# Kernel tuning notes

Measured on AMD Instinct MI355X. Metric: run time of the kernel, lower is better.

## Reference

```python
import jax, jax.numpy as jnp
import numpy as np

# ----- config (mirrors SpatialAxis init) -----
B, N = 1, 32768
D_MODEL, NHEAD, DEPTH = 256, 8, 2
COORD = 3
PATCH = 512          # self.patch_size default
BITS = 10            # self.morton_bits default
SHIFT = True         # self.shift_order default
MLP_H = 4 * D_MODEL
HD = D_MODEL // NHEAD
EPS = 1e-5


def _part1by2(v):
    # spread low 10 bits of int32 so there are 2 zero bits between each
    v = v & 0x000003FF
    v = (v | (v << 16)) & 0x030000FF
    v = (v | (v << 8)) & 0x0300F00F
    v = (v | (v << 4)) & 0x030C30C3
    v = (v | (v << 2)) & 0x09249249
    return v


def _perm_for_block(coords, i):
    # Z-order (Morton) serialization with per-block axis rotation; odd blocks
    # shift the order by half a patch (shifted-window style). Returns [B,N] int32.
    c = jax.lax.stop_gradient(coords)[..., np.roll(np.arange(COORD), -i)]
    cmin = c.min(axis=1, keepdims=True)
    cmax = c.max(axis=1, keepdims=True)
    q = ((c - cmin) / (cmax - cmin + 1e-9) * (2 ** BITS - 1)).astype(jnp.int32)
    q = jnp.clip(q, 0, 2 ** BITS - 1)
    code = (_part1by2(q[..., 0]) | (_part1by2(q[..., 1]) << 1)
            | (_part1by2(q[..., 2]) << 2))  # [B,N]
    perm = jnp.argsort(code, axis=1)
    if SHIFT and (i % 2 == 1):
        perm = jnp.roll(perm, PATCH // 2, axis=1)
    return perm


def _ln(x, g, b):
    m = x.mean(-1, keepdims=True)
    v = x.var(-1, keepdims=True)
    return (x - m) * jax.lax.rsqrt(v + EPS) * g + b


def _point_block(xs, cs, p):
    # xs: [M, P, D] tokens of one patch each; cs: [M, P, 3]
    M, P, D = xs.shape
    h = _ln(xs, p['ln1_g'], p['ln1_b'])
    qkv = h @ p['w_qkv'] + p['b_qkv']                         # [M,P,3D]
    q, k, v = jnp.split(qkv, 3, axis=-1)
    q = q.reshape(M, P, NHEAD, HD)
    k = k.reshape(M, P, NHEAD, HD)
    v = v.reshape(M, P, NHEAD, HD)
    scores = jnp.einsum('mphd,mqhd->mhpq', q, k) / np.sqrt(HD).astype(np.float32)
    rel = cs[:, :, None, :] - cs[:, None, :, :]               # [M,P,P,3]
    bias = jnp.einsum('mpqc,ch->mhpq', rel, p['w_pos']) + p['b_pos'][None, :, None, None]
    attn = jax.nn.softmax(scores + bias, axis=-1)
    o = jnp.einsum('mhpq,mqhd->mphd', attn, v).reshape(M, P, D)
    xs = xs + o @ p['w_proj'] + p['b_proj']
    h2 = _ln(xs, p['ln2_g'], p['ln2_b'])
    xs = xs + jax.nn.gelu(h2 @ p['w_fc1'] + p['b_fc1']) @ p['w_fc2'] + p['b_fc2']
    return xs


def _forward(x, coords, params):
    Cc = coords.shape[-1]
    nblk = N // PATCH
    for i in range(DEPTH):
        p = {k: v[i] for k, v in params.items()}
        perm = _perm_for_block(coords, i)                      # [B,N]
        inv = jnp.argsort(perm, axis=1)
        x_s = jnp.take_along_axis(x, perm[:, :, None], axis=1)
        c_s = jnp.take_along_axis(coords, perm[:, :, None], axis=1)
        x_f = x_s.reshape(B * nblk, PATCH, D_MODEL)
        c_f = c_s.reshape(B * nblk, PATCH, Cc)
        y = _point_block(x_f, c_f, p).reshape(B, N, D_MODEL)
        x = jnp.take_along_axis(y, inv[:, :, None], axis=1)
    return _ln(x, params['norm_g'][0], params['norm_b'][0])


def setup_inputs() -> dict:
    key = jax.random.key(0)
    ks = jax.random.split(key, 20)
    s = 0.02
    d = {
        'x': jax.random.normal(ks[0], (B, N, D_MODEL), jnp.float32),
        'coords': jax.random.uniform(ks[1], (B, N, COORD), jnp.float32),
        'ln1_g': jnp.ones((DEPTH, D_MODEL), jnp.float32),
        'ln1_b': jnp.zeros((DEPTH, D_MODEL), jnp.float32),
        'w_qkv': jax.random.normal(ks[2], (DEPTH, D_MODEL, 3 * D_MODEL), jnp.float32) * s,
        'b_qkv': jnp.zeros((DEPTH, 3 * D_MODEL), jnp.float32),
        'w_proj': jax.random.normal(ks[3], (DEPTH, D_MODEL, D_MODEL), jnp.float32) * s,
        'b_proj': jnp.zeros((DEPTH, D_MODEL), jnp.float32),
        'w_pos': jax.random.normal(ks[4], (DEPTH, COORD, NHEAD), jnp.float32) * s,
        'b_pos': jnp.zeros((DEPTH, NHEAD), jnp.float32),
        'ln2_g': jnp.ones((DEPTH, D_MODEL), jnp.float32),
        'ln2_b': jnp.zeros((DEPTH, D_MODEL), jnp.float32),
        'w_fc1': jax.random.normal(ks[5], (DEPTH, D_MODEL, MLP_H), jnp.float32) * s,
        'b_fc1': jnp.zeros((DEPTH, MLP_H), jnp.float32),
        'w_fc2': jax.random.normal(ks[6], (DEPTH, MLP_H, D_MODEL), jnp.float32) * s,
        'b_fc2': jnp.zeros((DEPTH, D_MODEL), jnp.float32),
        'norm_g': jnp.ones((1, D_MODEL), jnp.float32),
        'norm_b': jnp.zeros((1, D_MODEL), jnp.float32),
    }
    return d


def reference(x, coords, ln1_g, ln1_b, w_qkv, b_qkv, w_proj, b_proj, w_pos, b_pos,
              ln2_g, ln2_b, w_fc1, b_fc1, w_fc2, b_fc2, norm_g, norm_b):
    params = dict(ln1_g=ln1_g, ln1_b=ln1_b, w_qkv=w_qkv, b_qkv=b_qkv,
                  w_proj=w_proj, b_proj=b_proj, w_pos=w_pos, b_pos=b_pos,
                  ln2_g=ln2_g, ln2_b=ln2_b, w_fc1=w_fc1, b_fc1=b_fc1,
                  w_fc2=w_fc2, b_fc2=b_fc2, norm_g=norm_g, norm_b=norm_b)
    return _forward(x, coords, params)
```

## Files before the change

kernel.cpp:

```cpp
#include <hip/hip_runtime.h>

typedef unsigned long long u64;
typedef unsigned int u32;
typedef unsigned short u16;
typedef float f32x4 __attribute__((ext_vector_type(4)));
typedef __bf16 bf16x8 __attribute__((ext_vector_type(8)));

#define N_TOK 32768

__device__ inline u16 f2bf(float f){
  u32 x = __float_as_uint(f);
  u32 r = x + 0x7FFFu + ((x >> 16) & 1u);
  return (u16)(r >> 16);
}

__device__ inline u16 f2bf_hw(float f){
  u32 pk;
  asm("v_cvt_pk_bf16_f32 %0, %1, %2" : "=v"(pk) : "v"(f), "v"(0.f));
  return (u16)pk;
}

__device__ inline f32x4 mfma16(bf16x8 a, bf16x8 b, f32x4 c){
  return __builtin_amdgcn_mfma_f32_16x16x32_bf16(a, b, c, 0, 0, 0);
}

__device__ inline float fexp2(float x){
  float r;
  asm("v_exp_f32 %0, %1" : "=v"(r) : "v"(x));
  return r;
}
__device__ inline float frcp(float x){
  float r;
  asm("v_rcp_f32 %0, %1" : "=v"(r) : "v"(x));
  return r;
}

typedef const __attribute__((address_space(1))) unsigned int* gas_ptr;
typedef __attribute__((address_space(3))) unsigned int* las_ptr;
__device__ inline void gload_lds16(const u16* g, u16* l){
  __builtin_amdgcn_global_load_lds((gas_ptr)g, (las_ptr)l, 16, 0, 0);
}

__device__ inline u32 rp_idx(const u64* __restrict__ keys, int j, int shift){
  return (u32)(keys[(j + N_TOK - shift) & (N_TOK - 1)] & 0xFFFFull);
}

__device__ inline float gelu_tanh(float x){
  float u = 0.7978845608028654f * (x + 0.044715f * x * x * x);
  float e = fexp2(2.8853900817779268f * u);
  return 0.5f * x * (2.0f - 2.0f * frcp(e + 1.0f));
}

__device__ inline u32 part1by2(u32 v){
  v &= 0x3FFu;
  v = (v | (v << 16)) & 0x030000FFu;
  v = (v | (v << 8))  & 0x0300F00Fu;
  v = (v | (v << 4))  & 0x030C30C3u;
  v = (v | (v << 2))  & 0x09249249u;
  return v;
}

__device__ inline void ce64(u64& a, u64& b, bool asc){
  u64 lo = a < b ? a : b;
  u64 hi = a < b ? b : a;
  a = asc ? lo : hi;
  b = asc ? hi : lo;
}

__global__ void minmax_init(u32* __restrict__ cmm){
  int t = threadIdx.x;
  if (t < 3) cmm[t] = 0xFFFFFFFFu;
  else if (t < 6) cmm[t] = 0u;
}

__global__ void __launch_bounds__(256) minmax_atomic(const float* __restrict__ coords,
                                                     u32* __restrict__ cmm){
  __shared__ u32 smn[3], smx[3];
  int t = threadIdx.x;
  if (t < 3){ smn[t] = 0xFFFFFFFFu; smx[t] = 0u; }
  __syncthreads();
  int i = blockIdx.x * 256 + t;
  u32 bits = __float_as_uint(coords[i]);
  int a = i % 3;
  atomicMin(&smn[a], bits);
  atomicMax(&smx[a], bits);
  __syncthreads();
  if (t < 3){
    atomicMin(&cmm[t], smn[t]);
    atomicMax(&cmm[3 + t], smx[t]);
  }
}

__global__ void __launch_bounds__(256) wprep_kernel(const float* __restrict__ src,
                                                    u16* __restrict__ dst, int K, int Nn){
  int layer = blockIdx.y;
  src += (size_t)layer * K * Nn;
  dst += (size_t)layer * K * Nn;
  int ntx = Nn >> 5;
  int tk = blockIdx.x / ntx, tn = blockIdx.x % ntx;
  __shared__ float tile[32][33];
  int r = threadIdx.x >> 5, c = threadIdx.x & 31;
  for (int rr = r; rr < 32; rr += 8)
    tile[rr][c] = src[(size_t)(tk*32 + rr) * Nn + tn*32 + c];
  __syncthreads();
  for (int rr = r; rr < 32; rr += 8)
    dst[(size_t)(tn*32 + rr) * K + tk*32 + c] = f2bf(tile[c][rr]);
}

__global__ void __launch_bounds__(256) codes_kernel(const float* __restrict__ coords,
                                                    const float* __restrict__ cmm,
                                                    u64* __restrict__ keys){
  int p = blockIdx.x * 256 + threadIdx.x;
  int layer = p >> 15, t = p & (N_TOK - 1);
  u32 code = 0;
  #pragma unroll
  for (int j = 0; j < 3; ++j){
    int ax = (j + layer) % 3;
    float c = coords[t*3 + ax];
    float mn = cmm[ax], mx = cmm[3 + ax];
    float v = (c - mn) / (mx - mn + 1e-9f) * 1023.0f;
    int q = (int)v;
    q = q < 0 ? 0 : (q > 1023 ? 1023 : q);
    code |= part1by2((u32)q) << j;
  }
  keys[p] = ((u64)code << 16) | (u32)t;
}

__global__ void __launch_bounds__(64) sort_wave1024(u64* __restrict__ keys){
  int chunk = blockIdx.x;
  int lane = threadIdx.x;
  int base = chunk * 1024 + lane * 16;
  int bl = base & (N_TOK - 1);
  u64 v[16];
  #pragma unroll
  for (int p = 0; p < 16; ++p) v[p] = keys[base + p];
  #pragma unroll
  for (int k2 = 2; k2 <= 16; k2 <<= 1){
    #pragma unroll
    for (int j = k2 >> 1; j > 0; j >>= 1){
      #pragma unroll
      for (int p = 0; p < 16; ++p){
        if ((p & j) == 0){
          bool asc = (((bl + p) & k2) == 0);
          ce64(v[p], v[p+j], asc);
        }
      }
    }
  }
  #pragma unroll
  for (int kk = 32; kk <= 1024; kk <<= 1){
    bool asc = ((bl & kk) == 0);
    #pragma unroll
    for (int j = kk >> 1; j >= 16; j >>= 1){
      int m = j >> 4;
      bool kmin = asc != ((lane & m) != 0);
      #pragma unroll
      for (int p = 0; p < 16; ++p){
        u64 pv = __shfl_xor(v[p], m);
        u64 mn = v[p] < pv ? v[p] : pv;
        u64 mx = v[p] < pv ? pv : v[p];
        v[p] = kmin ? mn : mx;
      }
    }
    #pragma unroll
    for (int j = 8; j > 0; j >>= 1)
      #pragma unroll
      for (int p = 0; p < 16; ++p)
        if ((p & j) == 0) ce64(v[p], v[p+j], asc);
  }
  #pragma unroll
  for (int p = 0; p < 16; ++p) keys[base + p] = v[p];
}

template<int R>
__global__ void __launch_bounds__(256) sort_strided(u64* __restrict__ keys, int logJ, int k){
  const int E = 1 << R;
  int gps = N_TOK >> R;
  int tid = blockIdx.x * 256 + threadIdx.x;
  int seg = tid / gps, gamma = tid % gps;
  int high = gamma >> logJ, low = gamma & ((1 << logJ) - 1);
  int base = seg * N_TOK + (high << (logJ + R)) + low;
  u64 v[E];
  #pragma unroll
  for (int m = 0; m < E; ++m) v[m] = keys[base + (m << logJ)];
  bool asc = (((base & (N_TOK - 1)) & k) == 0);
  #pragma unroll
  for (int jj = R - 1; jj >= 0; --jj)
    #pragma unroll
    for (int m = 0; m < E; ++m)
      if ((m & (1 << jj)) == 0) ce64(v[m], v[m + (1 << jj)], asc);
  #pragma unroll
  for (int m = 0; m < E; ++m) keys[base + (m << logJ)] = v[m];
}

__global__ void __launch_bounds__(64) sort_tail1024(u64* __restrict__ keys, int k){
  int chunk = blockIdx.x;
  int lane = threadIdx.x;
  int base = chunk * 1024 + lane * 16;
  bool asc = ((((chunk * 1024) & (N_TOK - 1)) & k) == 0);
  u64 v[16];
  #pragma unroll
  for (int p = 0; p < 16; ++p) v[p] = keys[base + p];
  #pragma unroll
  for (int m = 32; m >= 1; m >>= 1){
    bool kmin = asc != ((lane & m) != 0);
    #pragma unroll
    for (int p = 0; p < 16; ++p){
      u64 pv = __shfl_xor(v[p], m);
      u64 mn = v[p] < pv ? v[p] : pv;
      u64 mx = v[p] < pv ? pv : v[p];
      v[p] = kmin ? mn : mx;
    }
  }
  #pragma unroll
  for (int j = 8; j > 0; j >>= 1)
    #pragma unroll
    for (int p = 0; p < 16; ++p)
      if ((p & j) == 0) ce64(v[p], v[p+j], asc);
  #pragma unroll
  for (int p = 0; p < 16; ++p) keys[base + p] = v[p];
}

__global__ void __launch_bounds__(256) gather_ln1_kernel(
    const float* __restrict__ xin, const float* __restrict__ coords,
    const u64* __restrict__ keys, int shift,
    const float* __restrict__ g1, const float* __restrict__ b1,
    const float* __restrict__ wpos,
    float* __restrict__ dproj, u16* __restrict__ h){
  int w = threadIdx.x >> 6, lane = threadIdx.x & 63;
  int j = blockIdx.x * 4 + w;
  u32 src = rp_idx(keys, j, shift);
  float4 v = ((const float4*)xin)[(size_t)src * 64 + lane];
  float s = v.x + v.y + v.z + v.w;
  for (int m = 1; m < 64; m <<= 1) s += __shfl_xor(s, m);
  float mean = s * (1.0f / 256.0f);
  float dx = v.x - mean, dy = v.y - mean, dz = v.z - mean, dw = v.w - mean;
  float q = dx*dx + dy*dy + dz*dz + dw*dw;
  for (int m = 1; m < 64; m <<= 1) q += __shfl_xor(q, m);
  float rs = rsqrtf(q * (1.0f / 256.0f) + 1e-5f);
  int c0 = lane * 4;
  u16 h0 = f2bf(dx * rs * g1[c0+0] + b1[c0+0]);
  u16 h1 = f2bf(dy * rs * g1[c0+1] + b1[c0+1]);
  u16 h2 = f2bf(dz * rs * g1[c0+2] + b1[c0+2]);
  u16 h3 = f2bf(dw * rs * g1[c0+3] + b1[c0+3]);
  uint2 pk; pk.x = (u32)h0 | ((u32)h1 << 16); pk.y = (u32)h2 | ((u32)h3 << 16);
  *(uint2*)&h[(size_t)j * 256 + c0] = pk;
  if (lane < 8){
    float acc = 0.0f;
    #pragma unroll
    for (int c = 0; c < 3; ++c) acc += coords[(size_t)src*3 + c] * wpos[c*8 + lane];
    dproj[(size_t)j * 8 + lane] = acc;
  }
}

__global__ void __launch_bounds__(256) ln_bf16_kernel(const float* __restrict__ xin,
    const float* __restrict__ g, const float* __restrict__ b, u16* __restrict__ out){
  int w = threadIdx.x >> 6, lane = threadIdx.x & 63;
  int j = blockIdx.x * 4 + w;
  float4 v = ((const float4*)xin)[(size_t)j * 64 + lane];
  float s = v.x + v.y + v.z + v.w;
  for (int m = 1; m < 64; m <<= 1) s += __shfl_xor(s, m);
  float mean = s * (1.0f / 256.0f);
  float dx = v.x - mean, dy = v.y - mean, dz = v.z - mean, dw = v.w - mean;
  float q = dx*dx + dy*dy + dz*dz + dw*dw;
  for (int m = 1; m < 64; m <<= 1) q += __shfl_xor(q, m);
  float rs = rsqrtf(q * (1.0f / 256.0f) + 1e-5f);
  int c0 = lane * 4;
  u16 h0 = f2bf(dx * rs * g[c0+0] + b[c0+0]);
  u16 h1 = f2bf(dy * rs * g[c0+1] + b[c0+1]);
  u16 h2 = f2bf(dz * rs * g[c0+2] + b[c0+2]);
  u16 h3 = f2bf(dw * rs * g[c0+3] + b[c0+3]);
  uint2 pk; pk.x = (u32)h0 | ((u32)h1 << 16); pk.y = (u32)h2 | ((u32)h3 << 16);
  *(uint2*)&out[(size_t)j * 256 + c0] = pk;
}

__global__ void __launch_bounds__(256) ln_final_kernel(const float* __restrict__ xin,
    const float* __restrict__ g, const float* __restrict__ b, float* __restrict__ out){
  int w = threadIdx.x >> 6, lane = threadIdx.x & 63;
  int j = blockIdx.x * 4 + w;
  float4 v = ((const float4*)xin)[(size_t)j * 64 + lane];
  float s = v.x + v.y + v.z + v.w;
  for (int m = 1; m < 64; m <<= 1) s += __shfl_xor(s, m);
  float mean = s * (1.0f / 256.0f);
  float dx = v.x - mean, dy = v.y - mean, dz = v.z - mean, dw = v.w - mean;
  float q = dx*dx + dy*dy + dz*dz + dw*dw;
  for (int m = 1; m < 64; m <<= 1) q += __shfl_xor(q, m);
  float rs = rsqrtf(q * (1.0f / 256.0f) + 1e-5f);
  int c0 = lane * 4;
  float4 o;
  o.x = dx * rs * g[c0+0] + b[c0+0];
  o.y = dy * rs * g[c0+1] + b[c0+1];
  o.z = dz * rs * g[c0+2] + b[c0+2];
  o.w = dw * rs * g[c0+3] + b[c0+3];
  ((float4*)out)[(size_t)j * 64 + lane] = o;
}

template<int EPI>
__global__ void __launch_bounds__(256) gemm_kernel(
    const u16* __restrict__ A, const u16* __restrict__ Wt,
    const float* __restrict__ bias, int K, int Nn,
    u16* __restrict__ outb, float* __restrict__ outf,
    const float* __restrict__ res, const u64* __restrict__ keys, int shift){
  __shared__ __align__(16) u16 As[2][128 * 32];
  __shared__ __align__(16) u16 Bs[2][128 * 32];
  int m0 = blockIdx.x * 128;
  int n0 = blockIdx.y * 128;
  int tid = threadIdx.x;
  int lane = tid & 63, lc = lane & 15, g = lane >> 4;
  int w = tid >> 6, wm = w >> 1, wn = w & 1;
  f32x4 acc[4][4];
  #pragma unroll
  for (int mi = 0; mi < 4; ++mi)
    #pragma unroll
    for (int ni = 0; ni < 4; ++ni) acc[mi][ni] = (f32x4){0.f,0.f,0.f,0.f};
  int r1 = tid >> 2, s1 = tid & 3;
  int r2 = r1 + 64;
  int sw = s1 ^ ((r1 >> 1) & 3);
  const u16* Ag1 = A  + (size_t)(m0 + r1) * K + sw*8;
  const u16* Ag2 = A  + (size_t)(m0 + r2) * K + sw*8;
  const u16* Bg1 = Wt + (size_t)(n0 + r1) * K + sw*8;
  const u16* Bg2 = Wt + (size_t)(n0 + r2) * K + sw*8;
  int wofs = (tid & ~63) * 8;
  int nt = K >> 5;
  gload_lds16(Ag1, As[0] + wofs);
  gload_lds16(Ag2, As[0] + wofs + 2048);
  gload_lds16(Bg1, Bs[0] + wofs);
  gload_lds16(Bg2, Bs[0] + wofs + 2048);
  int cur = 0;
  int fsw = (lc >> 1) & 3;
  for (int t = 0; t < nt; ++t){
    if (t + 1 < nt){
      int kk = (t + 1) << 5;
      gload_lds16(Ag1 + kk, As[cur^1] + wofs);
      gload_lds16(Ag2 + kk, As[cur^1] + wofs + 2048);
      gload_lds16(Bg1 + kk, Bs[cur^1] + wofs);
      gload_lds16(Bg2 + kk, Bs[cur^1] + wofs + 2048);
      asm volatile("s_waitcnt vmcnt(4)" ::: "memory");
    } else {
      asm volatile("s_waitcnt vmcnt(0)" ::: "memory");
    }
    __builtin_amdgcn_s_barrier();
    bf16x8 af[4], bfr[4];
    #pragma unroll
    for (int mi = 0; mi < 4; ++mi)
      af[mi] = *(const bf16x8*)&As[cur][(wm*64 + mi*16 + lc)*32 + (g ^ fsw)*8];
    #pragma unroll
    for (int ni = 0; ni < 4; ++ni)
      bfr[ni] = *(const bf16x8*)&Bs[cur][(wn*64 + ni*16 + lc)*32 + (g ^ fsw)*8];
    #pragma unroll
    for (int mi = 0; mi < 4; ++mi)
      #pragma unroll
      for (int ni = 0; ni < 4; ++ni)
        acc[mi][ni] = mfma16(af[mi], bfr[ni], acc[mi][ni]);
    asm volatile("" ::: "memory");
    __builtin_amdgcn_s_barrier();
    cur ^= 1;
  }
  #pragma unroll
  for (int ni = 0; ni < 4; ++ni){
    int col = n0 + wn*64 + ni*16 + lc;
    float bv = bias[col];
    #pragma unroll
    for (int mi = 0; mi < 4; ++mi){
      #pragma unroll
      for (int r = 0; r < 4; ++r){
        int row = m0 + wm*64 + mi*16 + g*4 + r;
        float v = acc[mi][ni][r] + bv;
        if constexpr (EPI == 0){
          if (col < 256) v *= 0.25500526f;
          outb[(size_t)row * Nn + col] = f2bf_hw(v);
        } else if constexpr (EPI == 1){
          outb[(size_t)row * Nn + col] = f2bf_hw(gelu_tanh(v));
        } else if constexpr (EPI == 2){
          u32 src = rp_idx(keys, row, shift);
          outf[(size_t)row * 256 + col] = res[(size_t)src * 256 + col] + v;
        } else {
          u32 dst = rp_idx(keys, row, shift);
          outf[(size_t)dst * 256 + col] = res[(size_t)row * 256 + col] + v;
        }
      }
    }
  }
}

#define VSTR 516
#define ATTN_LDS (512*32*2 + 32*VSTR*2 + 512*2)
__global__ void __launch_bounds__(512) attn_kernel(
    const u16* __restrict__ qkvb, const float* __restrict__ dproj,
    u16* __restrict__ o){
  extern __shared__ char smem[];
  u16* Kl = (u16*)smem;
  u16* Vt = (u16*)(smem + 512*32*2);
  u16* wl = (u16*)(smem + 512*32*2 + 32*VSTR*2);
  int h = blockIdx.x & 7;
  int base = (blockIdx.x >> 3) * 512;
  int tid = threadIdx.x, w = tid >> 6, lane = tid & 63, lc = lane & 15, g = lane >> 4;
  const float L2E = 1.4426950408889634f;
  for (int i = tid; i < 2048; i += 512){
    int j = i >> 2, s = i & 3;
    int swc = s ^ ((j >> 1) & 3);
    *(uint4*)&Kl[j*32 + s*8] =
      *(const uint4*)&qkvb[(size_t)(base + j)*768 + 256 + h*32 + swc*8];
  }
  for (int i = tid; i < 1024; i += 512){
    int p = i >> 2, d0 = (i & 3) * 8;
    int j0 = 2*p, j1 = j0 + 1;
    float wv0 = fexp2(-L2E * dproj[(size_t)(base + j0)*8 + h]);
    float wv1 = fexp2(-L2E * dproj[(size_t)(base + j1)*8 + h]);
    uint4 r0 = *(const uint4*)&qkvb[(size_t)(base + j0)*768 + 512 + h*32 + d0];
    uint4 r1 = *(const uint4*)&qkvb[(size_t)(base + j1)*768 + 512 + h*32 + d0];
    const u16* p0 = (const u16*)&r0; const u16* p1 = (const u16*)&r1;
    int j5 = j0 & 31, b = j5 >> 4, m = j5 & 15;
    int slot = (j0 & ~31) + 8*(m >> 2) + 4*b + (m & 3);
    #pragma unroll
    for (int e = 0; e < 8; ++e){
      float f0 = __uint_as_float(((u32)p0[e]) << 16) * wv0;
      float f1 = __uint_as_float(((u32)p1[e]) << 16) * wv1;
      u32 pk;
      asm("v_cvt_pk_bf16_f32 %0, %1, %2" : "=v"(pk) : "v"(f0), "v"(f1));
      *(u32*)&Vt[(d0 + e)*VSTR + slot] = pk;
    }
    if (d0 == 0){
      u32 pkw;
      asm("v_cvt_pk_bf16_f32 %0, %1, %2" : "=v"(pkw) : "v"(wv0), "v"(wv1));
      *(u32*)&wl[slot] = pkw;
    }
  }
  __syncthreads();
  const f32x4 zf = {0.f,0.f,0.f,0.f};
  const bf16x8 zb = {};
  const u16* Qg = qkvb + (size_t)base*768 + h*32;
  int fswk = (lc >> 1) & 3;
  for (int t = 0; t < 4; ++t){
    int q0 = w*64 + t*16;
    bf16x8 qf = *(const bf16x8*)&Qg[(size_t)(q0 + lc)*768 + g*8];
    f32x4 o0 = zf, o1 = zf, lacc = zf;
    #pragma unroll 4
    for (int grp = 0; grp < 16; ++grp){
      int kb = grp * 32;
      bf16x8 kf0 = *(const bf16x8*)&Kl[(kb + lc)*32 + (g ^ fswk)*8];
      bf16x8 kf1 = *(const bf16x8*)&Kl[(kb + 16 + lc)*32 + (g ^ fswk)*8];
      f32x4 s0 = mfma16(kf0, qf, zf);
      f32x4 s1 = mfma16(kf1, qf, zf);
      #pragma unroll
      for (int r = 0; r < 4; ++r){
        s0[r] = fexp2(s0[r]);
        s1[r] = fexp2(s1[r]);
      }
      u32 pk0, pk1, pk2, pk3;
      asm("v_cvt_pk_bf16_f32 %0, %1, %2" : "=v"(pk0) : "v"(s0[0]), "v"(s0[1]));
      asm("v_cvt_pk_bf16_f32 %0, %1, %2" : "=v"(pk1) : "v"(s0[2]), "v"(s0[3]));
      asm("v_cvt_pk_bf16_f32 %0, %1, %2" : "=v"(pk2) : "v"(s1[0]), "v"(s1[1]));
      asm("v_cvt_pk_bf16_f32 %0, %1, %2" : "=v"(pk3) : "v"(s1[2]), "v"(s1[3]));
      bf16x8 pf;
      ((u32*)&pf)[0] = pk0; ((u32*)&pf)[1] = pk1;
      ((u32*)&pf)[2] = pk2; ((u32*)&pf)[3] = pk3;
      bf16x8 v0, v1;
      *(uint2*)&v0       = *(const uint2*)&Vt[lc*VSTR + kb + g*8];
      *((uint2*)&v0 + 1) = *(const uint2*)&Vt[lc*VSTR + kb + g*8 + 4];
      *(uint2*)&v1       = *(const uint2*)&Vt[(16+lc)*VSTR + kb + g*8];
      *((uint2*)&v1 + 1) = *(const uint2*)&Vt[(16+lc)*VSTR + kb + g*8 + 4];
      bf16x8 wf = *(const bf16x8*)&wl[kb + g*8];
      bf16x8 wfz = (lc == 0) ? wf : zb;
      __builtin_amdgcn_s_setprio(1);
      o0 = mfma16(pf, v0, o0);
      o1 = mfma16(pf, v1, o1);
      lacc = mfma16(pf, wfz, lacc);
      __builtin_amdgcn_s_setprio(0);
    }
    #pragma unroll
    for (int r = 0; r < 4; ++r){
      float l = __shfl(lacc[r], lane & 48);
      float inv = 1.0f / l;
      size_t tok = (size_t)(base + q0 + g*4 + r);
      o[tok*256 + h*32 + lc]      = f2bf(o0[r] * inv);
      o[tok*256 + h*32 + 16 + lc] = f2bf(o1[r] * inv);
    }
  }
}

extern "C" void kernel_launch(void* const* d_in, const int* in_sizes, int n_in,
                              void* d_out, int out_size, void* d_ws, size_t ws_size,
                              hipStream_t stream){
  const float* x      = (const float*)d_in[0];
  const float* coords = (const float*)d_in[1];
  const float* ln1_g  = (const float*)d_in[2];
  const float* ln1_b  = (const float*)d_in[3];
  const float* w_qkv  = (const float*)d_in[4];
  const float* b_qkv  = (const float*)d_in[5];
  const float* w_proj = (const float*)d_in[6];
  const float* b_proj = (const float*)d_in[7];
  const float* w_pos  = (const float*)d_in[8];
  const float* ln2_g  = (const float*)d_in[10];
  const float* ln2_b  = (const float*)d_in[11];
  const float* w_fc1  = (const float*)d_in[12];
  const float* b_fc1  = (const float*)d_in[13];
  const float* w_fc2  = (const float*)d_in[14];
  const float* b_fc2  = (const float*)d_in[15];
  const float* norm_g = (const float*)d_in[16];
  const float* norm_b = (const float*)d_in[17];
  float* outp = (float*)d_out;

  hipFuncSetAttribute((const void*)attn_kernel,
                      hipFuncAttributeMaxDynamicSharedMemorySize, ATTN_LDS);

  char* ws = (char*)d_ws;
  size_t off = 0;
  auto alloc = [&](size_t bytes) -> void* {
    void* p = ws + off;
    off += (bytes + 255) & ~(size_t)255;
    return p;
  };
  u64*   keys   = (u64*)  alloc((size_t)2 * N_TOK * 8);
  float* cmm    = (float*)alloc(256);
  float* dproj  = (float*)alloc((size_t)N_TOK * 8 * 4);
  u16*   h      = (u16*)  alloc((size_t)N_TOK * 256 * 2);
  u16*   qkvb   = (u16*)  alloc((size_t)N_TOK * 768 * 2);
  float* x2     = (float*)alloc((size_t)N_TOK * 256 * 4);
  u16*   t      = (u16*)  alloc((size_t)N_TOK * 1024 * 2);
  float* xA     = (float*)alloc((size_t)N_TOK * 256 * 4);
  u16*   wtqkv  = (u16*)  alloc((size_t)2 * 256 * 768 * 2);
  u16*   wtproj = (u16*)  alloc((size_t)2 * 256 * 256 * 2);
  u16*   wtfc1  = (u16*)  alloc((size_t)2 * 256 * 1024 * 2);
  u16*   wtfc2  = (u16*)  alloc((size_t)2 * 1024 * 256 * 2);
  u16*   o      = t;
  float* xB     = (float*)qkvb;
  (void)in_sizes; (void)n_in; (void)out_size; (void)ws_size;

  minmax_init<<<1, 64, 0, stream>>>((u32*)cmm);
  minmax_atomic<<<384, 256, 0, stream>>>(coords, (u32*)cmm);
  wprep_kernel<<<dim3(8*24, 2),  256, 0, stream>>>(w_qkv,  wtqkv,  256, 768);
  wprep_kernel<<<dim3(8*8, 2),   256, 0, stream>>>(w_proj, wtproj, 256, 256);
  wprep_kernel<<<dim3(8*32, 2),  256, 0, stream>>>(w_fc1,  wtfc1,  256, 1024);
  wprep_kernel<<<dim3(32*8, 2),  256, 0, stream>>>(w_fc2,  wtfc2,  1024, 256);

  codes_kernel<<<256, 256, 0, stream>>>(coords, cmm, keys);
  sort_wave1024<<<64, 64, 0, stream>>>(keys);
  sort_strided<1><<<128, 256, 0, stream>>>(keys, 10, 2048);
  sort_tail1024<<<64, 64, 0, stream>>>(keys, 2048);
  sort_strided<2><<<64, 256, 0, stream>>>(keys, 10, 4096);
  sort_tail1024<<<64, 64, 0, stream>>>(keys, 4096);
  sort_strided<3><<<32, 256, 0, stream>>>(keys, 10, 8192);
  sort_tail1024<<<64, 64, 0, stream>>>(keys, 8192);
  sort_strided<3><<<32, 256, 0, stream>>>(keys, 11, 16384);
  sort_strided<1><<<128, 256, 0, stream>>>(keys, 10, 16384);
  sort_tail1024<<<64, 64, 0, stream>>>(keys, 16384);
  sort_strided<3><<<32, 256, 0, stream>>>(keys, 12, 32768);
  sort_strided<2><<<64, 256, 0, stream>>>(keys, 10, 32768);
  sort_tail1024<<<64, 64, 0, stream>>>(keys, 32768);

  for (int layer = 0; layer < 2; ++layer){
    int shift = (layer & 1) ? 256 : 0;
    const float* xin = (layer == 0) ? x : xA;
    float* xout = (layer == 0) ? xA : xB;
    u64* keyL = keys + (size_t)layer * N_TOK;

    gather_ln1_kernel<<<8192, 256, 0, stream>>>(xin, coords, keyL, shift,
        ln1_g + layer*256, ln1_b + layer*256, w_pos + layer*24, dproj, h);
    gemm_kernel<0><<<dim3(256, 6), 256, 0, stream>>>(h, wtqkv + (size_t)layer*768*256,
        b_qkv + layer*768, 256, 768, qkvb, nullptr, nullptr, nullptr, 0);
    attn_kernel<<<512, 512, ATTN_LDS, stream>>>(qkvb, dproj, o);
    gemm_kernel<2><<<dim3(256, 2), 256, 0, stream>>>(o, wtproj + (size_t)layer*256*256,
        b_proj + layer*256, 256, 256, nullptr, x2, xin, keyL, shift);
    ln_bf16_kernel<<<8192, 256, 0, stream>>>(x2, ln2_g + layer*256, ln2_b + layer*256, h);
    gemm_kernel<1><<<dim3(256, 8), 256, 0, stream>>>(h, wtfc1 + (size_t)layer*1024*256,
        b_fc1 + layer*1024, 256, 1024, t, nullptr, nullptr, nullptr, 0);
    gemm_kernel<3><<<dim3(256, 2), 256, 0, stream>>>(t, wtfc2 + (size_t)layer*256*1024,
        b_fc2 + layer*256, 1024, 256, nullptr, xout, x2, keyL, shift);
  }
  ln_final_kernel<<<8192, 256, 0, stream>>>(xB, norm_g, norm_b, outp);
}
```

Before: 501.1 us.

## Triple-buffer GEMM LDS pipeline and stage bf16 epilogue through LDS

The GEMM main loop moves from double to triple buffering in one shared LDS array, issuing loads two k-tiles ahead with matching vmcnt waits so global latency is hidden better. For the bf16-output epilogues (QKV and FC1 with GELU), results are written into an LDS tile first and then stored as coalesced 16-byte row chunks, replacing scattered 2-byte global stores. This costs more LDS per block (48KB), which may lower occupancy. The residual/permute epilogues keep their old path.

```diff
diff --git a/kernel.cpp b/kernel.cpp
--- a/kernel.cpp
+++ b/kernel.cpp
@@ -301,8 +301,7 @@
     const float* __restrict__ bias, int K, int Nn,
     u16* __restrict__ outb, float* __restrict__ outf,
     const float* __restrict__ res, const u64* __restrict__ keys, int shift){
-  __shared__ __align__(16) u16 As[2][128 * 32];
-  __shared__ __align__(16) u16 Bs[2][128 * 32];
+  __shared__ __align__(16) u16 smem[3 * 8192];
   int m0 = blockIdx.x * 128;
   int n0 = blockIdx.y * 128;
   int tid = threadIdx.x;
@@ -322,31 +321,38 @@
   const u16* Bg2 = Wt + (size_t)(n0 + r2) * K + sw*8;
   int wofs = (tid & ~63) * 8;
   int nt = K >> 5;
-  gload_lds16(Ag1, As[0] + wofs);
-  gload_lds16(Ag2, As[0] + wofs + 2048);
-  gload_lds16(Bg1, Bs[0] + wofs);
-  gload_lds16(Bg2, Bs[0] + wofs + 2048);
-  int cur = 0;
+  auto issue = [&](int t, int b){
+    int kk = t << 5;
+    u16* Ab = smem + b * 8192;
+    gload_lds16(Ag1 + kk, Ab + wofs);
+    gload_lds16(Ag2 + kk, Ab + wofs + 2048);
+    gload_lds16(Bg1 + kk, Ab + 4096 + wofs);
+    gload_lds16(Bg2 + kk, Ab + 4096 + wofs + 2048);
+  };
+  issue(0, 0);
+  issue(1, 1);
+  int b0 = 0;
   int fsw = (lc >> 1) & 3;
   for (int t = 0; t < nt; ++t){
-    if (t + 1 < nt){
-      int kk = (t + 1) << 5;
-      gload_lds16(Ag1 + kk, As[cur^1] + wofs);
-      gload_lds16(Ag2 + kk, As[cur^1] + wofs + 2048);
-      gload_lds16(Bg1 + kk, Bs[cur^1] + wofs);
-      gload_lds16(Bg2 + kk, Bs[cur^1] + wofs + 2048);
+    int b2 = b0 + 2; if (b2 >= 3) b2 -= 3;
+    if (t + 2 < nt){
+      issue(t + 2, b2);
+      asm volatile("s_waitcnt vmcnt(8)" ::: "memory");
+    } else if (t + 1 < nt){
       asm volatile("s_waitcnt vmcnt(4)" ::: "memory");
     } else {
       asm volatile("s_waitcnt vmcnt(0)" ::: "memory");
     }
     __builtin_amdgcn_s_barrier();
+    const u16* Asb = smem + b0 * 8192;
+    const u16* Bsb = Asb + 4096;
     bf16x8 af[4], bfr[4];
     #pragma unroll
     for (int mi = 0; mi < 4; ++mi)
-      af[mi] = *(const bf16x8*)&As[cur][(wm*64 + mi*16 + lc)*32 + (g ^ fsw)*8];
+      af[mi] = *(const bf16x8*)&Asb[(wm*64 + mi*16 + lc)*32 + (g ^ fsw)*8];
     #pragma unroll
     for (int ni = 0; ni < 4; ++ni)
-      bfr[ni] = *(const bf16x8*)&Bs[cur][(wn*64 + ni*16 + lc)*32 + (g ^ fsw)*8];
+      bfr[ni] = *(const bf16x8*)&Bsb[(wn*64 + ni*16 + lc)*32 + (g ^ fsw)*8];
     #pragma unroll
     for (int mi = 0; mi < 4; ++mi)
       #pragma unroll
@@ -354,29 +360,56 @@
         acc[mi][ni] = mfma16(af[mi], bfr[ni], acc[mi][ni]);
     asm volatile("" ::: "memory");
     __builtin_amdgcn_s_barrier();
-    cur ^= 1;
-  }
-  #pragma unroll
-  for (int ni = 0; ni < 4; ++ni){
-    int col = n0 + wn*64 + ni*16 + lc;
-    float bv = bias[col];
-    #pragma unroll
-    for (int mi = 0; mi < 4; ++mi){
+    b0 = b0 + 1; if (b0 >= 3) b0 -= 3;
+  }
+  if constexpr (EPI == 0 || EPI == 1){
+    u16* Ct = smem;
+    #pragma unroll
+    for (int ni = 0; ni < 4; ++ni){
+      int col = n0 + wn*64 + ni*16 + lc;
+      float bv = bias[col];
       #pragma unroll
-      for (int r = 0; r < 4; ++r){
-        int row = m0 + wm*64 + mi*16 + g*4 + r;
-        float v = acc[mi][ni][r] + bv;
-        if constexpr (EPI == 0){
-          if (col < 256) v *= 0.25500526f;
-          outb[(size_t)row * Nn + col] = f2bf_hw(v);
-        } else if constexpr (EPI == 1){
-          outb[(size_t)row * Nn + col] = f2bf_hw(gelu_tanh(v));
-        } else if constexpr (EPI == 2){
-          u32 src = rp_idx(keys, row, shift);
-          outf[(size_t)row * 256 + col] = res[(size_t)src * 256 + col] + v;
-        } else {
-          u32 dst = rp_idx(keys, row, shift);
-          outf[(size_t)dst * 256 + col] = res[(size_t)row * 256 + col] + v;
+      for (int mi = 0; mi < 4; ++mi){
+        #pragma unroll
+        for (int r = 0; r < 4; ++r){
+          int lrow = wm*64 + mi*16 + g*4 + r;
+          float v = acc[mi][ni][r] + bv;
+          if constexpr (EPI == 0){
+            if (col < 256) v *= 0.25500526f;
+          } else {
+            v = gelu_tanh(v);
+          }
+          Ct[lrow*136 + wn*64 + ni*16 + lc] = f2bf_hw(v);
+        }
+      }
+    }
+    __syncthreads();
+    int row = tid >> 1, half = tid & 1;
+    const uint4* srcp = (const uint4*)&Ct[row*136 + half*64];
+    uint4 d[8];
+    #pragma unroll
+    for (int i = 0; i < 8; ++i) d[i] = srcp[i];
+    uint4* dstp = (uint4*)(outb + (size_t)(m0 + row) * Nn + n0 + half*64);
+    #pragma unroll
+    for (int i = 0; i < 8; ++i) dstp[i] = d[i];
+  } else {
+    #pragma unroll
+    for (int ni = 0; ni < 4; ++ni){
+      int col = n0 + wn*64 + ni*16 + lc;
+      float bv = bias[col];
+      #pragma unroll
+      for (int mi = 0; mi < 4; ++mi){
+        #pragma unroll
+        for (int r = 0; r < 4; ++r){
+          int row = m0 + wm*64 + mi*16 + g*4 + r;
+          float v = acc[mi][ni][r] + bv;
+          if constexpr (EPI == 2){
+            u32 src = rp_idx(keys, row, shift);
+            outf[(size_t)row * 256 + col] = res[(size_t)src * 256 + col] + v;
+          } else {
+            u32 dst = rp_idx(keys, row, shift);
+            outf[(size_t)dst * 256 + col] = res[(size_t)row * 256 + col] + v;
+          }
         }
       }
     }
```

Result: slower. 514.7 us (+2.7%).

## Add larger-tile 1024-thread GEMM for QKV, FC1 and FC2 projections

Applied to the files above, without the earlier changes.

Introduces a second GEMM kernel with 256-row tiles (256 or 128 columns) and 16 waves per block, and routes the QKV, FC1 and FC2 matmuls through it. The old kernel keeps only the proj epilogue. Larger tiles raise data reuse per LDS load and halve the grid, cutting global traffic for A and weights. The cost is fewer blocks (384–512 for 256 CUs), more LDS per block and possibly lower occupancy and worse tail balance. FC2 with K=1024 gets only 256 blocks.

```diff
diff --git a/kernel.cpp b/kernel.cpp
--- a/kernel.cpp
+++ b/kernel.cpp
@@ -295,6 +295,96 @@
   ((float4*)out)[(size_t)j * 64 + lane] = o;
 }
 
+template<int EPI, int BN>
+__global__ void __launch_bounds__(1024) gemm2_kernel(
+    const u16* __restrict__ A, const u16* __restrict__ Wt,
+    const float* __restrict__ bias, int K, int Nn,
+    u16* __restrict__ outb, float* __restrict__ outf,
+    const float* __restrict__ res, const u64* __restrict__ keys, int shift){
+  constexpr int WN = (BN == 256) ? 4 : 2;
+  constexpr int WM = 16 / WN;
+  constexpr int MI = (256 / WM) / 16;
+  constexpr int NI = (BN / WN) / 16;
+  constexpr int SPANM = 256 / WM;
+  constexpr int SPANN = BN / WN;
+  __shared__ __align__(16) u16 As[2][256 * 32];
+  __shared__ __align__(16) u16 Bs[2][BN * 32];
+  int m0 = blockIdx.x * 256;
+  int n0 = blockIdx.y * BN;
+  int tid = threadIdx.x;
+  int lane = tid & 63, lc = lane & 15, g = lane >> 4;
+  int w = tid >> 6;
+  int wm = (BN == 256) ? (w >> 2) : (w >> 1);
+  int wn = (BN == 256) ? (w & 3) : (w & 1);
+  f32x4 acc[MI][NI];
+  #pragma unroll
+  for (int mi = 0; mi < MI; ++mi)
+    #pragma unroll
+    for (int ni = 0; ni < NI; ++ni) acc[mi][ni] = (f32x4){0.f,0.f,0.f,0.f};
+  int rA = tid >> 2, sA = tid & 3;
+  const u16* Ag = A + (size_t)(m0 + rA) * K + (sA ^ ((rA >> 1) & 3)) * 8;
+  int cb = (BN == 256) ? tid : (tid & 511);
+  int rB = cb >> 2, sB = cb & 3;
+  const u16* Bg = Wt + (size_t)(n0 + rB) * K + (sB ^ ((rB >> 1) & 3)) * 8;
+  int aofs = (tid & ~63) * 8;
+  int bofs = (cb & ~63) * 8;
+  int nt = K >> 5;
+  auto issue = [&](int t, int b){
+    int kk = t << 5;
+    gload_lds16(Ag + kk, As[b] + aofs);
+    gload_lds16(Bg + kk, Bs[b] + bofs);
+  };
+  issue(0, 0);
+  int cur = 0;
+  int fsw = (lc >> 1) & 3;
+  for (int t = 0; t < nt; ++t){
+    if (t + 1 < nt){
+      issue(t + 1, cur ^ 1);
+      asm volatile("s_waitcnt vmcnt(2)" ::: "memory");
+    } else {
+      asm volatile("s_waitcnt vmcnt(0)" ::: "memory");
+    }
+    __builtin_amdgcn_s_barrier();
+    bf16x8 af[MI], bfr[NI];
+    #pragma unroll
+    for (int mi = 0; mi < MI; ++mi)
+      af[mi] = *(const bf16x8*)&As[cur][(wm*SPANM + mi*16 + lc)*32 + (g ^ fsw)*8];
+    #pragma unroll
+    for (int ni = 0; ni < NI; ++ni)
+      bfr[ni] = *(const bf16x8*)&Bs[cur][(wn*SPANN + ni*16 + lc)*32 + (g ^ fsw)*8];
+    #pragma unroll
+    for (int mi = 0; mi < MI; ++mi)
+      #pragma unroll
+      for (int ni = 0; ni < NI; ++ni)
+        acc[mi][ni] = mfma16(af[mi], bfr[ni], acc[mi][ni]);
+    asm volatile("" ::: "memory");
+    __builtin_amdgcn_s_barrier();
+    cur ^= 1;
+  }
+  #pragma unroll
+  for (int ni = 0; ni < NI; ++ni){
+    int col = n0 + wn*SPANN + ni*16 + lc;
+    float bv = bias[col];
+    #pragma unroll
+    for (int mi = 0; mi < MI; ++mi){
+      #pragma unroll
+      for (int r = 0; r < 4; ++r){
+        int row = m0 + wm*SPANM + mi*16 + g*4 + r;
+        float v = acc[mi][ni][r] + bv;
+        if constexpr (EPI == 0){
+          if (col < 256) v *= 0.25500526f;
+          outb[(size_t)row * Nn + col] = f2bf_hw(v);
+        } else if constexpr (EPI == 1){
+          outb[(size_t)row * Nn + col] = f2bf_hw(gelu_tanh(v));
+        } else {
+          u32 dst = rp_idx(keys, row, shift);
+          outf[(size_t)dst * 256 + col] = res[(size_t)row * 256 + col] + v;
+        }
+      }
+    }
+  }
+}
+
 template<int EPI>
 __global__ void __launch_bounds__(256) gemm_kernel(
     const u16* __restrict__ A, const u16* __restrict__ Wt,
@@ -366,17 +456,11 @@
       for (int r = 0; r < 4; ++r){
         int row = m0 + wm*64 + mi*16 + g*4 + r;
         float v = acc[mi][ni][r] + bv;
-        if constexpr (EPI == 0){
-          if (col < 256) v *= 0.25500526f;
-          outb[(size_t)row * Nn + col] = f2bf_hw(v);
-        } else if constexpr (EPI == 1){
-          outb[(size_t)row * Nn + col] = f2bf_hw(gelu_tanh(v));
-        } else if constexpr (EPI == 2){
+        if constexpr (EPI == 2){
           u32 src = rp_idx(keys, row, shift);
           outf[(size_t)row * 256 + col] = res[(size_t)src * 256 + col] + v;
         } else {
-          u32 dst = rp_idx(keys, row, shift);
-          outf[(size_t)dst * 256 + col] = res[(size_t)row * 256 + col] + v;
+          outb[(size_t)row * Nn + col] = f2bf_hw(v);
         }
       }
     }
@@ -557,15 +641,15 @@
 
     gather_ln1_kernel<<<8192, 256, 0, stream>>>(xin, coords, keyL, shift,
         ln1_g + layer*256, ln1_b + layer*256, w_pos + layer*24, dproj, h);
-    gemm_kernel<0><<<dim3(256, 6), 256, 0, stream>>>(h, wtqkv + (size_t)layer*768*256,
+    gemm2_kernel<0,256><<<dim3(128, 3), 1024, 0, stream>>>(h, wtqkv + (size_t)layer*768*256,
         b_qkv + layer*768, 256, 768, qkvb, nullptr, nullptr, nullptr, 0);
     attn_kernel<<<512, 512, ATTN_LDS, stream>>>(qkvb, dproj, o);
     gemm_kernel<2><<<dim3(256, 2), 256, 0, stream>>>(o, wtproj + (size_t)layer*256*256,
         b_proj + layer*256, 256, 256, nullptr, x2, xin, keyL, shift);
     ln_bf16_kernel<<<8192, 256, 0, stream>>>(x2, ln2_g + layer*256, ln2_b + layer*256, h);
-    gemm_kernel<1><<<dim3(256, 8), 256, 0, stream>>>(h, wtfc1 + (size_t)layer*1024*256,
+    gemm2_kernel<1,256><<<dim3(128, 4), 1024, 0, stream>>>(h, wtfc1 + (size_t)layer*1024*256,
         b_fc1 + layer*1024, 256, 1024, t, nullptr, nullptr, nullptr, 0);
-    gemm_kernel<3><<<dim3(256, 2), 256, 0, stream>>>(t, wtfc2 + (size_t)layer*256*1024,
+    gemm2_kernel<3,128><<<dim3(128, 2), 1024, 0, stream>>>(t, wtfc2 + (size_t)layer*256*1024,
         b_fc2 + layer*256, 1024, 256, nullptr, xout, x2, keyL, shift);
   }
   ln_final_kernel<<<8192, 256, 0, stream>>>(xB, norm_g, norm_b, outp);
```

Result: faster. 490.2 us (-2.2%).
